# Kernel tuning notes

Measured on AMD Instinct MI355X. Metric: run time of the kernel, lower is better.

Reference implementation:

```python
import jax, jax.numpy as jnp
import numpy as np
from jax import lax

CURRICULUM_EP = 12
LI, LS, LW = 0.5, 0.8, 3.0


def _gauss_win(ws, C, dtype):
    coords = jnp.arange(ws, dtype=jnp.float32) - ws // 2
    g = jnp.exp(-coords ** 2 / (2 * 1.5 ** 2))
    win = g[None, :] * g[:, None]
    win = win / win.sum()
    # depthwise kernel, OIHW with I=1, O=C
    return jnp.broadcast_to(win[None, None], (C, 1, ws, ws)).astype(dtype)


def _dwconv(x, win, p, C):
    return lax.conv_general_dilated(
        x, win, window_strides=(1, 1), padding=[(p, p), (p, p)],
        dimension_numbers=('NCHW', 'OIHW', 'NCHW'), feature_group_count=C)


def diff_ssim(x, y, ws=11):
    C1, C2 = 0.01 ** 2, 0.03 ** 2
    C = x.shape[1]
    p = ws // 2
    win = _gauss_win(ws, C, x.dtype)
    mx = _dwconv(x, win, p, C)
    my = _dwconv(y, win, p, C)
    sxx = _dwconv(x * x, win, p, C) - mx ** 2
    syy = _dwconv(y * y, win, p, C) - my ** 2
    sxy = _dwconv(x * y, win, p, C) - mx * my
    ssim_map = (2 * mx * my + C1) * (2 * sxy + C2) / ((mx ** 2 + my ** 2 + C1) * (sxx + syy + C2))
    return ssim_map.mean()


def setup_inputs() -> dict:
    key = jax.random.key(0)
    k1, k2, k3, k4 = jax.random.split(key, 4)
    B, C, H, W = 16, 3, 512, 512
    NB = 1024  # watermark bits
    eps = 1e-4
    cover = jax.random.uniform(k1, (B, C, H, W), dtype=jnp.float32)
    wmed = jax.random.uniform(k2, (B, C, H, W), dtype=jnp.float32)
    wm_orig = jax.random.uniform(k3, (B, NB), dtype=jnp.float32)
    wm_ext = jnp.clip(jax.random.uniform(k4, (B, NB), dtype=jnp.float32), eps, 1.0 - eps)
    return {"cover": cover, "wmed": wmed, "wm_orig": wm_orig, "wm_ext": wm_ext, "epoch": 20}


def reference(cover, wmed, wm_orig, wm_ext, epoch):
    ml = jnp.mean((wmed - cover) ** 2)
    sv = diff_ssim(wmed, cover)
    sl = 1.0 - sv
    wl = jnp.mean(-(wm_orig * jnp.log(wm_ext) + (1.0 - wm_orig) * jnp.log(1.0 - wm_ext)))
    if epoch <= CURRICULUM_EP:
        w_img, w_ssim = 0.05, 0.05
    else:
        progress = min(1.0, (epoch - CURRICULUM_EP) / 10.0)
        w_img = 0.05 + (LI - 0.05) * progress
        w_ssim = 0.05 + (LS - 0.05) * progress
    total = w_img * ml + w_ssim * sl + LW * wl
    return (total, ml, sv, wl)
```

## Files before the change

kernel.cpp:

```cpp
#include <hip/hip_runtime.h>
#include <math.h>

#define H_IMG 512
#define W_IMG 512
#define TW 32
#define CH 32
#define NCHUNK 4
#define STRIP (CH*NCHUNK)
#define HALO 5
#define WS11 11
#define RING 42
#define RS 36
#define FSTR (RING*RS)
#define NTHREADS 256

typedef float f2 __attribute__((ext_vector_type(2)));

__host__ __device__ constexpr float WT(int t) {
    return (t==0||t==10) ? 0.00102838f :
           (t==1||t==9)  ? 0.00759873f :
           (t==2||t==8)  ? 0.03600075f :
           (t==3||t==7)  ? 0.10936070f :
           (t==4||t==6)  ? 0.21300556f :
           (t==5)        ? 0.26601172f : 0.0f;
}

static __device__ __forceinline__ f2 splat2(float v) { f2 r = {v, v}; return r; }

__global__ __launch_bounds__(NTHREADS, 5) void ssim_mse_tile(
        const float* __restrict__ cover, const float* __restrict__ wmed,
        float* __restrict__ part, int nParts) {
    __shared__ __align__(16) float rbuf[5*FSTR];

    const int tid = threadIdx.x;
    const int bx  = blockIdx.x & 15;
    const int ys  = (blockIdx.x >> 4) & 3;
    const int pl  = blockIdx.x >> 6;
    const size_t pbase = (size_t)pl * (H_IMG*W_IMG);
    const float* xp = wmed + pbase;
    const float* yp = cover + pbase;
    const int Y0  = ys << 7;
    const int tx0 = bx*TW - HALO;
    const bool xin = (bx != 0) && (bx != 15);

    float ssim_acc = 0.f, mse_acc = 0.f;

    for (int k = 0; k < NCHUNK; ++k) {
        const int nrows = (k == 0) ? (CH + 2*HALO) : CH;
        const int hr0   = (k == 0) ? -HALO : (CH*k + HALO);
        const int ntask = nrows << 3;

        for (int t = tid; t < ntask; t += NTHREADS) {
            const int r  = t >> 3, c0 = (t & 7) << 2;
            const int hr = hr0 + r;
            const int gy = Y0 + hr;
            const int slot = (hr + HALO) % RING;
            const bool rok = (unsigned)gy < (unsigned)H_IMG;
            float xv[14], yv[14];
            if (rok && xin) {
                const int ga = tx0 + c0 - 3;
                const float* rx = xp + (size_t)gy*W_IMG + ga;
                const float* ry = yp + (size_t)gy*W_IMG + ga;
                float4 XA = *(const float4*)(rx);
                float4 XB = *(const float4*)(rx + 4);
                float4 XC = *(const float4*)(rx + 8);
                float4 XD = *(const float4*)(rx + 12);
                float  XE = rx[16];
                float4 YA = *(const float4*)(ry);
                float4 YB = *(const float4*)(ry + 4);
                float4 YC = *(const float4*)(ry + 8);
                float4 YD = *(const float4*)(ry + 12);
                float  YE = ry[16];
                xv[0]=XA.w;  xv[1]=XB.x;  xv[2]=XB.y;  xv[3]=XB.z;  xv[4]=XB.w;
                xv[5]=XC.x;  xv[6]=XC.y;  xv[7]=XC.z;  xv[8]=XC.w;  xv[9]=XD.x;
                xv[10]=XD.y; xv[11]=XD.z; xv[12]=XD.w; xv[13]=XE;
                yv[0]=YA.w;  yv[1]=YB.x;  yv[2]=YB.y;  yv[3]=YB.z;  yv[4]=YB.w;
                yv[5]=YC.x;  yv[6]=YC.y;  yv[7]=YC.z;  yv[8]=YC.w;  yv[9]=YD.x;
                yv[10]=YD.y; yv[11]=YD.z; yv[12]=YD.w; yv[13]=YE;
            } else if (rok) {
                const int gc = tx0 + c0;
                const float* prx = xp + (size_t)gy*W_IMG + gc;
                const float* pry = yp + (size_t)gy*W_IMG + gc;
#pragma unroll
                for (int j = 0; j < 14; ++j) {
                    bool ok = (unsigned)(gc + j) < (unsigned)W_IMG;
                    xv[j] = ok ? prx[j] : 0.f;
                    yv[j] = ok ? pry[j] : 0.f;
                }
            } else {
#pragma unroll
                for (int j = 0; j < 14; ++j) { xv[j] = 0.f; yv[j] = 0.f; }
            }

            if ((unsigned)hr < (unsigned)STRIP) {
#pragma unroll
                for (int j = 5; j < 9; ++j) {
                    float d = xv[j] - yv[j];
                    mse_acc = fmaf(d, d, mse_acc);
                }
            }

            f2 A[5][2];
#pragma unroll
            for (int f = 0; f < 5; ++f) { A[f][0] = splat2(0.f); A[f][1] = splat2(0.f); }
#pragma unroll
            for (int j = 0; j < 14; ++j) {
                float px = xv[j], py = yv[j];
                float pxx = px*px, pyy = py*py, pxy = px*py;
#pragma unroll
                for (int p = 0; p < 2; ++p) {
                    const int t0 = j - 2*p;
                    if (t0 >= 0 && t0 <= WS11) {
                        const f2 wp = {WT(t0), WT(t0-1)};
                        A[0][p] = __builtin_elementwise_fma(wp, splat2(px),  A[0][p]);
                        A[1][p] = __builtin_elementwise_fma(wp, splat2(py),  A[1][p]);
                        A[2][p] = __builtin_elementwise_fma(wp, splat2(pxx), A[2][p]);
                        A[3][p] = __builtin_elementwise_fma(wp, splat2(pyy), A[3][p]);
                        A[4][p] = __builtin_elementwise_fma(wp, splat2(pxy), A[4][p]);
                    }
                }
            }
            float* wb = &rbuf[slot*RS + c0];
#pragma unroll
            for (int f = 0; f < 5; ++f) {
                *(float4*)(wb + f*FSTR) =
                    make_float4(A[f][0].x, A[f][0].y, A[f][1].x, A[f][1].y);
            }
        }
        __syncthreads();

        {
            const int c  = tid & 31;
            const int rg = tid >> 3 >> 2;
            const int sb = (CH*k + (rg << 2)) % RING;
            f2 acc[5][2];
#pragma unroll
            for (int f = 0; f < 5; ++f) {
                acc[f][0] = splat2(0.f); acc[f][1] = splat2(0.f);
            }
            const float* bp = rbuf + c;
#pragma unroll
            for (int i = 0; i < 14; ++i) {
                int sl = sb + i; if (sl >= RING) sl -= RING;
                const float* rp = bp + sl*RS;
#pragma unroll
                for (int f = 0; f < 5; ++f) {
                    float v = rp[f*FSTR];
#pragma unroll
                    for (int p = 0; p < 2; ++p) {
                        const int t0 = i - 2*p;
                        if (t0 >= 0 && t0 <= WS11) {
                            const f2 wp = {WT(t0), WT(t0-1)};
                            acc[f][p] = __builtin_elementwise_fma(wp, splat2(v), acc[f][p]);
                        }
                    }
                }
            }
            const f2 c1v = {1e-4f, 1e-4f};
            const f2 c2v = {9e-4f, 9e-4f};
            const f2 two = {2.f, 2.f};
#pragma unroll
            for (int p = 0; p < 2; ++p) {
                f2 mx = acc[0][p], my = acc[1][p];
                f2 sxx = acc[2][p] - mx*mx;
                f2 syy = acc[3][p] - my*my;
                f2 sxy = acc[4][p] - mx*my;
                f2 num = (two*mx*my + c1v) * (two*sxy + c2v);
                f2 den = (mx*mx + my*my + c1v) * (sxx + syy + c2v);
                ssim_acc += __fdividef(num.x, den.x) + __fdividef(num.y, den.y);
            }
        }
        __syncthreads();
    }

#pragma unroll
    for (int off = 32; off > 0; off >>= 1) {
        ssim_acc += __shfl_down(ssim_acc, off);
        mse_acc  += __shfl_down(mse_acc, off);
    }
    const int wid = tid >> 6, lane = tid & 63;
    if (lane == 0) { rbuf[wid] = ssim_acc; rbuf[4+wid] = mse_acc; }
    __syncthreads();
    if (tid == 0) {
        part[blockIdx.x] = rbuf[0]+rbuf[1]+rbuf[2]+rbuf[3];
        part[nParts + blockIdx.x] = rbuf[4]+rbuf[5]+rbuf[6]+rbuf[7];
    }
}

#define FT 1024
__global__ __launch_bounds__(FT) void finalize_k(
        const float* __restrict__ part, int nParts,
        const float* __restrict__ wm_orig, const float* __restrict__ wm_ext,
        int nWm, const int* __restrict__ epoch_p,
        float* __restrict__ out, double inv_npix, double inv_nwm) {
    __shared__ double red[48];
    int tid = threadIdx.x;
    double s_ssim = 0.0, s_mse = 0.0, s_wl = 0.0;
    const float4* s4 = (const float4*)part;
    const float4* m4 = (const float4*)(part + nParts);
    int n4 = nParts >> 2;
    for (int i = tid; i < n4; i += FT) {
        float4 v = s4[i];
        s_ssim += (double)((v.x + v.y) + (v.z + v.w));
        float4 u = m4[i];
        s_mse  += (double)((u.x + u.y) + (u.z + u.w));
    }
    const float4* p4 = (const float4*)wm_orig;
    const float4* q4 = (const float4*)wm_ext;
    int w4 = nWm >> 2;
    for (int i = tid; i < w4; i += FT) {
        float4 p = p4[i], q = q4[i];
        float a;
        a  = -(p.x*__logf(q.x) + (1.f-p.x)*__logf(1.f-q.x));
        a += -(p.y*__logf(q.y) + (1.f-p.y)*__logf(1.f-q.y));
        a += -(p.z*__logf(q.z) + (1.f-p.z)*__logf(1.f-q.z));
        a += -(p.w*__logf(q.w) + (1.f-p.w)*__logf(1.f-q.w));
        s_wl += (double)a;
    }
#pragma unroll
    for (int off = 32; off > 0; off >>= 1) {
        s_ssim += __shfl_down(s_ssim, off);
        s_mse  += __shfl_down(s_mse, off);
        s_wl   += __shfl_down(s_wl, off);
    }
    int wid = tid >> 6, lane = tid & 63;
    if (lane == 0) { red[wid] = s_ssim; red[16+wid] = s_mse; red[32+wid] = s_wl; }
    __syncthreads();
    if (tid == 0) {
        double ssim_sum = 0.0, mse_sum = 0.0, wl_sum = 0.0;
        for (int i = 0; i < 16; ++i) {
            ssim_sum += red[i]; mse_sum += red[16+i]; wl_sum += red[32+i];
        }
        float sv = (float)(ssim_sum * inv_npix);
        float ml = (float)(mse_sum  * inv_npix);
        float wl = (float)(wl_sum   * inv_nwm);
        int e = *epoch_p;
        float w_img, w_ssim;
        if (e <= 12) {
            w_img = 0.05f; w_ssim = 0.05f;
        } else {
            float progress = fminf(1.0f, (float)(e - 12) / 10.0f);
            w_img  = 0.05f + (0.5f - 0.05f)*progress;
            w_ssim = 0.05f + (0.8f - 0.05f)*progress;
        }
        float sl = 1.0f - sv;
        float total = w_img*ml + w_ssim*sl + 3.0f*wl;
        out[0] = total;
        out[1] = ml;
        out[2] = sv;
        out[3] = wl;
    }
}

extern "C" void kernel_launch(void* const* d_in, const int* in_sizes, int n_in,
                              void* d_out, int out_size, void* d_ws, size_t ws_size,
                              hipStream_t stream) {
    const float* cover   = (const float*)d_in[0];
    const float* wmed    = (const float*)d_in[1];
    const float* wm_orig = (const float*)d_in[2];
    const float* wm_ext  = (const float*)d_in[3];
    const int*   epoch   = (const int*)d_in[4];
    float* out = (float*)d_out;

    int npix   = in_sizes[0];
    int planes = npix / (H_IMG * W_IMG);
    int nWm    = in_sizes[2];

    int nBlocks = 16 * 4 * planes;
    int nParts  = nBlocks;
    float* part = (float*)d_ws;

    ssim_mse_tile<<<nBlocks, NTHREADS, 0, stream>>>(cover, wmed, part, nParts);
    finalize_k<<<1, FT, 0, stream>>>(part, nParts, wm_orig, wm_ext, nWm,
                                     epoch, out,
                                     1.0 / (double)npix, 1.0 / (double)nWm);
}
```

Measured before the change: 176.6 us.

## Prefetch next chunk's rows into registers while computing vertical SSIM pass

Restructures the per-chunk loop so global loads for the next chunk's rows are issued into registers before the vertical convolution and SSIM math of the current chunk, then consumed into the shared ring buffer afterward. The aim is to hide global memory latency behind compute. The prefetched row data raises register pressure, so launch bounds drop from 5 to 4 blocks per CU, reducing occupancy. The first chunk's 42 halo rows are also split explicitly over two load passes.

```diff
diff --git a/kernel.cpp b/kernel.cpp
--- a/kernel.cpp
+++ b/kernel.cpp
@@ -27,7 +27,105 @@
 
 static __device__ __forceinline__ f2 splat2(float v) { f2 r = {v, v}; return r; }
 
-__global__ __launch_bounds__(NTHREADS, 5) void ssim_mse_tile(
+struct Pre {
+    float4 XA, XB, XC, XD; float XE;
+    float4 YA, YB, YC, YD; float YE;
+};
+
+static __device__ __forceinline__ void issue_row(Pre& P,
+        const float* __restrict__ xp, const float* __restrict__ yp,
+        int gy, int tx0, int c0, bool xin, bool rok) {
+    if (!rok) return;
+    const size_t rowoff = (size_t)gy * W_IMG;
+    if (xin) {
+        const float* rx = xp + rowoff + (tx0 + c0 - 3);
+        const float* ry = yp + rowoff + (tx0 + c0 - 3);
+        P.XA = *(const float4*)(rx);
+        P.XB = *(const float4*)(rx + 4);
+        P.XC = *(const float4*)(rx + 8);
+        P.XD = *(const float4*)(rx + 12);
+        P.XE = rx[16];
+        P.YA = *(const float4*)(ry);
+        P.YB = *(const float4*)(ry + 4);
+        P.YC = *(const float4*)(ry + 8);
+        P.YD = *(const float4*)(ry + 12);
+        P.YE = ry[16];
+    } else {
+        const int gc = tx0 + c0;
+        const float* prx = xp + rowoff + gc;
+        const float* pry = yp + rowoff + gc;
+        float t[14], u[14];
+#pragma unroll
+        for (int j = 0; j < 14; ++j) {
+            bool ok = (unsigned)(gc + j) < (unsigned)W_IMG;
+            t[j] = ok ? prx[j] : 0.f;
+            u[j] = ok ? pry[j] : 0.f;
+        }
+        P.XA.w = t[0];
+        P.XB.x = t[1];  P.XB.y = t[2];  P.XB.z = t[3];  P.XB.w = t[4];
+        P.XC.x = t[5];  P.XC.y = t[6];  P.XC.z = t[7];  P.XC.w = t[8];
+        P.XD.x = t[9];  P.XD.y = t[10]; P.XD.z = t[11]; P.XD.w = t[12];
+        P.XE   = t[13];
+        P.YA.w = u[0];
+        P.YB.x = u[1];  P.YB.y = u[2];  P.YB.z = u[3];  P.YB.w = u[4];
+        P.YC.x = u[5];  P.YC.y = u[6];  P.YC.z = u[7];  P.YC.w = u[8];
+        P.YD.x = u[9];  P.YD.y = u[10]; P.YD.z = u[11]; P.YD.w = u[12];
+        P.YE   = u[13];
+    }
+}
+
+static __device__ __forceinline__ void consume_row(const Pre& P,
+        float* __restrict__ wb, bool rok, bool own, float& mse_acc) {
+    if (!rok) {
+        const float4 z = make_float4(0.f, 0.f, 0.f, 0.f);
+#pragma unroll
+        for (int f = 0; f < 5; ++f) *(float4*)(wb + f*FSTR) = z;
+        return;
+    }
+    float xv[14], yv[14];
+    xv[0]=P.XA.w;  xv[1]=P.XB.x;  xv[2]=P.XB.y;  xv[3]=P.XB.z;  xv[4]=P.XB.w;
+    xv[5]=P.XC.x;  xv[6]=P.XC.y;  xv[7]=P.XC.z;  xv[8]=P.XC.w;  xv[9]=P.XD.x;
+    xv[10]=P.XD.y; xv[11]=P.XD.z; xv[12]=P.XD.w; xv[13]=P.XE;
+    yv[0]=P.YA.w;  yv[1]=P.YB.x;  yv[2]=P.YB.y;  yv[3]=P.YB.z;  yv[4]=P.YB.w;
+    yv[5]=P.YC.x;  yv[6]=P.YC.y;  yv[7]=P.YC.z;  yv[8]=P.YC.w;  yv[9]=P.YD.x;
+    yv[10]=P.YD.y; yv[11]=P.YD.z; yv[12]=P.YD.w; yv[13]=P.YE;
+
+    if (own) {
+#pragma unroll
+        for (int j = 5; j < 9; ++j) {
+            float d = xv[j] - yv[j];
+            mse_acc = fmaf(d, d, mse_acc);
+        }
+    }
+
+    f2 A[5][2];
+#pragma unroll
+    for (int f = 0; f < 5; ++f) { A[f][0] = splat2(0.f); A[f][1] = splat2(0.f); }
+#pragma unroll
+    for (int j = 0; j < 14; ++j) {
+        float px = xv[j], py = yv[j];
+        float pxx = px*px, pyy = py*py, pxy = px*py;
+#pragma unroll
+        for (int p = 0; p < 2; ++p) {
+            const int t0 = j - 2*p;
+            if (t0 >= 0 && t0 <= WS11) {
+                const f2 wp = {WT(t0), WT(t0-1)};
+                A[0][p] = __builtin_elementwise_fma(wp, splat2(px),  A[0][p]);
+                A[1][p] = __builtin_elementwise_fma(wp, splat2(py),  A[1][p]);
+                A[2][p] = __builtin_elementwise_fma(wp, splat2(pxx), A[2][p]);
+                A[3][p] = __builtin_elementwise_fma(wp, splat2(pyy), A[3][p]);
+                A[4][p] = __builtin_elementwise_fma(wp, splat2(pxy), A[4][p]);
+            }
+        }
+    }
+#pragma unroll
+    for (int f = 0; f < 5; ++f) {
+        *(float4*)(wb + f*FSTR) =
+            make_float4(A[f][0].x, A[f][0].y, A[f][1].x, A[f][1].y);
+    }
+}
+
+__global__ __launch_bounds__(NTHREADS, 4) void ssim_mse_tile(
         const float* __restrict__ cover, const float* __restrict__ wmed,
         float* __restrict__ part, int nParts) {
     __shared__ __align__(16) float rbuf[5*FSTR];
@@ -43,96 +141,36 @@
     const int tx0 = bx*TW - HALO;
     const bool xin = (bx != 0) && (bx != 15);
 
+    const int rA = tid >> 3;
+    const int c0 = (tid & 7) << 2;
+
     float ssim_acc = 0.f, mse_acc = 0.f;
+    Pre P;
+
+    {
+        Pre P0, P1;
+        const int  hrA  = rA - HALO;
+        const int  gyA  = Y0 + hrA;
+        const bool rokA = (unsigned)gyA < (unsigned)H_IMG;
+        const bool two  = (tid < 80);
+        const int  gyB  = gyA + 32;
+        const bool rokB = two && ((unsigned)gyB < (unsigned)H_IMG);
+        issue_row(P0, xp, yp, gyA, tx0, c0, xin, rokA);
+        if (two) issue_row(P1, xp, yp, gyB, tx0, c0, xin, rokB);
+        consume_row(P0, &rbuf[rA*RS + c0], rokA, hrA >= 0, mse_acc);
+        if (two) consume_row(P1, &rbuf[(rA+32)*RS + c0], rokB, true, mse_acc);
+        const int  gy1  = Y0 + CH + HALO + rA;
+        const bool rok1 = (unsigned)gy1 < (unsigned)H_IMG;
+        issue_row(P, xp, yp, gy1, tx0, c0, xin, rok1);
+    }
+    __syncthreads();
+
+    int slotA = rA;
+    int sbB   = (tid >> 5) << 2;
 
     for (int k = 0; k < NCHUNK; ++k) {
-        const int nrows = (k == 0) ? (CH + 2*HALO) : CH;
-        const int hr0   = (k == 0) ? -HALO : (CH*k + HALO);
-        const int ntask = nrows << 3;
-
-        for (int t = tid; t < ntask; t += NTHREADS) {
-            const int r  = t >> 3, c0 = (t & 7) << 2;
-            const int hr = hr0 + r;
-            const int gy = Y0 + hr;
-            const int slot = (hr + HALO) % RING;
-            const bool rok = (unsigned)gy < (unsigned)H_IMG;
-            float xv[14], yv[14];
-            if (rok && xin) {
-                const int ga = tx0 + c0 - 3;
-                const float* rx = xp + (size_t)gy*W_IMG + ga;
-                const float* ry = yp + (size_t)gy*W_IMG + ga;
-                float4 XA = *(const float4*)(rx);
-                float4 XB = *(const float4*)(rx + 4);
-                float4 XC = *(const float4*)(rx + 8);
-                float4 XD = *(const float4*)(rx + 12);
-                float  XE = rx[16];
-                float4 YA = *(const float4*)(ry);
-                float4 YB = *(const float4*)(ry + 4);
-                float4 YC = *(const float4*)(ry + 8);
-                float4 YD = *(const float4*)(ry + 12);
-                float  YE = ry[16];
-                xv[0]=XA.w;  xv[1]=XB.x;  xv[2]=XB.y;  xv[3]=XB.z;  xv[4]=XB.w;
-                xv[5]=XC.x;  xv[6]=XC.y;  xv[7]=XC.z;  xv[8]=XC.w;  xv[9]=XD.x;
-                xv[10]=XD.y; xv[11]=XD.z; xv[12]=XD.w; xv[13]=XE;
-                yv[0]=YA.w;  yv[1]=YB.x;  yv[2]=YB.y;  yv[3]=YB.z;  yv[4]=YB.w;
-                yv[5]=YC.x;  yv[6]=YC.y;  yv[7]=YC.z;  yv[8]=YC.w;  yv[9]=YD.x;
-                yv[10]=YD.y; yv[11]=YD.z; yv[12]=YD.w; yv[13]=YE;
-            } else if (rok) {
-                const int gc = tx0 + c0;
-                const float* prx = xp + (size_t)gy*W_IMG + gc;
-                const float* pry = yp + (size_t)gy*W_IMG + gc;
-#pragma unroll
-                for (int j = 0; j < 14; ++j) {
-                    bool ok = (unsigned)(gc + j) < (unsigned)W_IMG;
-                    xv[j] = ok ? prx[j] : 0.f;
-                    yv[j] = ok ? pry[j] : 0.f;
-                }
-            } else {
-#pragma unroll
-                for (int j = 0; j < 14; ++j) { xv[j] = 0.f; yv[j] = 0.f; }
-            }
-
-            if ((unsigned)hr < (unsigned)STRIP) {
-#pragma unroll
-                for (int j = 5; j < 9; ++j) {
-                    float d = xv[j] - yv[j];
-                    mse_acc = fmaf(d, d, mse_acc);
-                }
-            }
-
-            f2 A[5][2];
-#pragma unroll
-            for (int f = 0; f < 5; ++f) { A[f][0] = splat2(0.f); A[f][1] = splat2(0.f); }
-#pragma unroll
-            for (int j = 0; j < 14; ++j) {
-                float px = xv[j], py = yv[j];
-                float pxx = px*px, pyy = py*py, pxy = px*py;
-#pragma unroll
-                for (int p = 0; p < 2; ++p) {
-                    const int t0 = j - 2*p;
-                    if (t0 >= 0 && t0 <= WS11) {
-                        const f2 wp = {WT(t0), WT(t0-1)};
-                        A[0][p] = __builtin_elementwise_fma(wp, splat2(px),  A[0][p]);
-                        A[1][p] = __builtin_elementwise_fma(wp, splat2(py),  A[1][p]);
-                        A[2][p] = __builtin_elementwise_fma(wp, splat2(pxx), A[2][p]);
-                        A[3][p] = __builtin_elementwise_fma(wp, splat2(pyy), A[3][p]);
-                        A[4][p] = __builtin_elementwise_fma(wp, splat2(pxy), A[4][p]);
-                    }
-                }
-            }
-            float* wb = &rbuf[slot*RS + c0];
-#pragma unroll
-            for (int f = 0; f < 5; ++f) {
-                *(float4*)(wb + f*FSTR) =
-                    make_float4(A[f][0].x, A[f][0].y, A[f][1].x, A[f][1].y);
-            }
-        }
-        __syncthreads();
-
         {
-            const int c  = tid & 31;
-            const int rg = tid >> 3 >> 2;
-            const int sb = (CH*k + (rg << 2)) % RING;
+            const int c = tid & 31;
             f2 acc[5][2];
 #pragma unroll
             for (int f = 0; f < 5; ++f) {
@@ -141,7 +179,7 @@
             const float* bp = rbuf + c;
 #pragma unroll
             for (int i = 0; i < 14; ++i) {
-                int sl = sb + i; if (sl >= RING) sl -= RING;
+                int sl = sbB + i; if (sl >= RING) sl -= RING;
                 const float* rp = bp + sl*RS;
 #pragma unroll
                 for (int f = 0; f < 5; ++f) {
@@ -158,20 +196,36 @@
             }
             const f2 c1v = {1e-4f, 1e-4f};
             const f2 c2v = {9e-4f, 9e-4f};
-            const f2 two = {2.f, 2.f};
+            const f2 two2 = {2.f, 2.f};
 #pragma unroll
             for (int p = 0; p < 2; ++p) {
                 f2 mx = acc[0][p], my = acc[1][p];
                 f2 sxx = acc[2][p] - mx*mx;
                 f2 syy = acc[3][p] - my*my;
                 f2 sxy = acc[4][p] - mx*my;
-                f2 num = (two*mx*my + c1v) * (two*sxy + c2v);
+                f2 num = (two2*mx*my + c1v) * (two2*sxy + c2v);
                 f2 den = (mx*mx + my*my + c1v) * (sxx + syy + c2v);
                 ssim_acc += __fdividef(num.x, den.x) + __fdividef(num.y, den.y);
             }
         }
-        __syncthreads();
-    }
+
+        if (k + 1 < NCHUNK) {
+            __syncthreads();
+            const int  hr  = CH*(k+1) + HALO + rA;
+            const int  gy  = Y0 + hr;
+            const bool rok = (unsigned)gy < (unsigned)H_IMG;
+            consume_row(P, &rbuf[slotA*RS + c0], rok, hr < STRIP, mse_acc);
+            if (k + 2 < NCHUNK) {
+                const int  gy2  = gy + CH;
+                const bool rok2 = (unsigned)gy2 < (unsigned)H_IMG;
+                issue_row(P, xp, yp, gy2, tx0, c0, xin, rok2);
+            }
+            slotA += CH; if (slotA >= RING) slotA -= RING;
+            sbB   += CH; if (sbB   >= RING) sbB   -= RING;
+            __syncthreads();
+        }
+    }
+    __syncthreads();
 
 #pragma unroll
     for (int off = 32; off > 0; off >>= 1) {
```

Measured after the change: 198.8 us. 12.5% more time.

## Prefetch next chunk rows into registers and overlap loads with vertical pass

Applied to the files above, without the earlier changes.

Restructures the strip loop so each thread register-prefetches the global rows for the next chunk while the vertical convolution and SSIM of the current chunk run. The prologue fills the halo rows separately, and the per-chunk horizontal pass now reads the prefetched registers. Barriers become a custom s_waitcnt lgkmcnt plus s_barrier, and the occupancy hint drops from 5 to 4 waves to make room for the extra live registers. The aim is to hide global load latency behind compute, at the cost of more register pressure and lower occupancy.

```diff
diff --git a/kernel.cpp b/kernel.cpp
--- a/kernel.cpp
+++ b/kernel.cpp
@@ -16,6 +16,11 @@
 
 typedef float f2 __attribute__((ext_vector_type(2)));
 
+#define BAR() do { \
+    asm volatile("s_waitcnt lgkmcnt(0)" ::: "memory"); \
+    __builtin_amdgcn_s_barrier(); \
+} while (0)
+
 __host__ __device__ constexpr float WT(int t) {
     return (t==0||t==10) ? 0.00102838f :
            (t==1||t==9)  ? 0.00759873f :
@@ -27,7 +32,7 @@
 
 static __device__ __forceinline__ f2 splat2(float v) { f2 r = {v, v}; return r; }
 
-__global__ __launch_bounds__(NTHREADS, 5) void ssim_mse_tile(
+__global__ __launch_bounds__(NTHREADS, 4) void ssim_mse_tile(
         const float* __restrict__ cover, const float* __restrict__ wmed,
         float* __restrict__ part, int nParts) {
     __shared__ __align__(16) float rbuf[5*FSTR];
@@ -43,40 +48,166 @@
     const int tx0 = bx*TW - HALO;
     const bool xin = (bx != 0) && (bx != 15);
 
+    const int rA  = tid >> 3;
+    const int c0  = (tid & 7) << 2;
+    const int cB  = tid & 31;
+    const int rgB = tid >> 5;
+
     float ssim_acc = 0.f, mse_acc = 0.f;
+    float4 pXA, pXB, pXC, pXD, pYA, pYB, pYC, pYD;
+    float  pXE, pYE;
+
+    for (int t = tid; t < 336; t += NTHREADS) {
+        const int r  = t >> 3, cc = (t & 7) << 2;
+        const int hr = r - HALO;
+        const int gy = Y0 + hr;
+        const bool rok = (unsigned)gy < (unsigned)H_IMG;
+        float xv[14], yv[14];
+        if (rok && xin) {
+            const float* rx = xp + (size_t)gy*W_IMG + (tx0 + cc - 3);
+            const float* ry = yp + (size_t)gy*W_IMG + (tx0 + cc - 3);
+            float4 XA = *(const float4*)(rx);
+            float4 XB = *(const float4*)(rx + 4);
+            float4 XC = *(const float4*)(rx + 8);
+            float4 XD = *(const float4*)(rx + 12);
+            float  XE = rx[16];
+            float4 YA = *(const float4*)(ry);
+            float4 YB = *(const float4*)(ry + 4);
+            float4 YC = *(const float4*)(ry + 8);
+            float4 YD = *(const float4*)(ry + 12);
+            float  YE = ry[16];
+            xv[0]=XA.w;  xv[1]=XB.x;  xv[2]=XB.y;  xv[3]=XB.z;  xv[4]=XB.w;
+            xv[5]=XC.x;  xv[6]=XC.y;  xv[7]=XC.z;  xv[8]=XC.w;  xv[9]=XD.x;
+            xv[10]=XD.y; xv[11]=XD.z; xv[12]=XD.w; xv[13]=XE;
+            yv[0]=YA.w;  yv[1]=YB.x;  yv[2]=YB.y;  yv[3]=YB.z;  yv[4]=YB.w;
+            yv[5]=YC.x;  yv[6]=YC.y;  yv[7]=YC.z;  yv[8]=YC.w;  yv[9]=YD.x;
+            yv[10]=YD.y; yv[11]=YD.z; yv[12]=YD.w; yv[13]=YE;
+        } else if (rok) {
+            const int gc = tx0 + cc;
+            const float* prx = xp + (size_t)gy*W_IMG + gc;
+            const float* pry = yp + (size_t)gy*W_IMG + gc;
+#pragma unroll
+            for (int j = 0; j < 14; ++j) {
+                bool ok = (unsigned)(gc + j) < (unsigned)W_IMG;
+                xv[j] = ok ? prx[j] : 0.f;
+                yv[j] = ok ? pry[j] : 0.f;
+            }
+        } else {
+#pragma unroll
+            for (int j = 0; j < 14; ++j) { xv[j] = 0.f; yv[j] = 0.f; }
+        }
+        if ((unsigned)hr < (unsigned)STRIP) {
+#pragma unroll
+            for (int j = 5; j < 9; ++j) {
+                float d = xv[j] - yv[j];
+                mse_acc = fmaf(d, d, mse_acc);
+            }
+        }
+        f2 A[5][2];
+#pragma unroll
+        for (int f = 0; f < 5; ++f) { A[f][0] = splat2(0.f); A[f][1] = splat2(0.f); }
+#pragma unroll
+        for (int j = 0; j < 14; ++j) {
+            float px = xv[j], py = yv[j];
+            float pxx = px*px, pyy = py*py, pxy = px*py;
+#pragma unroll
+            for (int p = 0; p < 2; ++p) {
+                const int t0 = j - 2*p;
+                if (t0 >= 0 && t0 <= WS11) {
+                    const f2 wp = {WT(t0), WT(t0-1)};
+                    A[0][p] = __builtin_elementwise_fma(wp, splat2(px),  A[0][p]);
+                    A[1][p] = __builtin_elementwise_fma(wp, splat2(py),  A[1][p]);
+                    A[2][p] = __builtin_elementwise_fma(wp, splat2(pxx), A[2][p]);
+                    A[3][p] = __builtin_elementwise_fma(wp, splat2(pyy), A[3][p]);
+                    A[4][p] = __builtin_elementwise_fma(wp, splat2(pxy), A[4][p]);
+                }
+            }
+        }
+        float* wb = &rbuf[r*RS + cc];
+#pragma unroll
+        for (int f = 0; f < 5; ++f) {
+            *(float4*)(wb + f*FSTR) =
+                make_float4(A[f][0].x, A[f][0].y, A[f][1].x, A[f][1].y);
+        }
+    }
+    if (xin) {
+        const int gy1 = Y0 + CH + HALO + rA;
+        const float* rx = xp + (size_t)gy1*W_IMG + (tx0 + c0 - 3);
+        const float* ry = yp + (size_t)gy1*W_IMG + (tx0 + c0 - 3);
+        pXA = *(const float4*)(rx);
+        pXB = *(const float4*)(rx + 4);
+        pXC = *(const float4*)(rx + 8);
+        pXD = *(const float4*)(rx + 12);
+        pXE = rx[16];
+        pYA = *(const float4*)(ry);
+        pYB = *(const float4*)(ry + 4);
+        pYC = *(const float4*)(ry + 8);
+        pYD = *(const float4*)(ry + 12);
+        pYE = ry[16];
+    }
+    BAR();
+
+    int slotA = rA;
+    int sbB   = rgB << 2;
 
     for (int k = 0; k < NCHUNK; ++k) {
-        const int nrows = (k == 0) ? (CH + 2*HALO) : CH;
-        const int hr0   = (k == 0) ? -HALO : (CH*k + HALO);
-        const int ntask = nrows << 3;
-
-        for (int t = tid; t < ntask; t += NTHREADS) {
-            const int r  = t >> 3, c0 = (t & 7) << 2;
-            const int hr = hr0 + r;
-            const int gy = Y0 + hr;
-            const int slot = (hr + HALO) % RING;
-            const bool rok = (unsigned)gy < (unsigned)H_IMG;
+        {
+            f2 acc[5][2];
+#pragma unroll
+            for (int f = 0; f < 5; ++f) {
+                acc[f][0] = splat2(0.f); acc[f][1] = splat2(0.f);
+            }
+            const float* bp = rbuf + cB;
+#pragma unroll
+            for (int i = 0; i < 14; ++i) {
+                int sl = sbB + i; if (sl >= RING) sl -= RING;
+                const float* rp = bp + sl*RS;
+#pragma unroll
+                for (int f = 0; f < 5; ++f) {
+                    float v = rp[f*FSTR];
+#pragma unroll
+                    for (int p = 0; p < 2; ++p) {
+                        const int t0 = i - 2*p;
+                        if (t0 >= 0 && t0 <= WS11) {
+                            const f2 wp = {WT(t0), WT(t0-1)};
+                            acc[f][p] = __builtin_elementwise_fma(wp, splat2(v), acc[f][p]);
+                        }
+                    }
+                }
+            }
+            const f2 c1v = {1e-4f, 1e-4f};
+            const f2 c2v = {9e-4f, 9e-4f};
+            const f2 two2 = {2.f, 2.f};
+#pragma unroll
+            for (int p = 0; p < 2; ++p) {
+                f2 mx = acc[0][p], my = acc[1][p];
+                f2 sxx = acc[2][p] - mx*mx;
+                f2 syy = acc[3][p] - my*my;
+                f2 sxy = acc[4][p] - mx*my;
+                f2 num = (two2*mx*my + c1v) * (two2*sxy + c2v);
+                f2 den = (mx*mx + my*my + c1v) * (sxx + syy + c2v);
+                ssim_acc += __fdividef(num.x, den.x) + __fdividef(num.y, den.y);
+            }
+        }
+
+        if (k + 1 < NCHUNK) {
+            BAR();
+            const int  hr  = CH*(k+1) + HALO + rA;
+            const int  gy  = Y0 + hr;
+            const bool rok = gy < H_IMG;
             float xv[14], yv[14];
-            if (rok && xin) {
-                const int ga = tx0 + c0 - 3;
-                const float* rx = xp + (size_t)gy*W_IMG + ga;
-                const float* ry = yp + (size_t)gy*W_IMG + ga;
-                float4 XA = *(const float4*)(rx);
-                float4 XB = *(const float4*)(rx + 4);
-                float4 XC = *(const float4*)(rx + 8);
-                float4 XD = *(const float4*)(rx + 12);
-                float  XE = rx[16];
-                float4 YA = *(const float4*)(ry);
-                float4 YB = *(const float4*)(ry + 4);
-                float4 YC = *(const float4*)(ry + 8);
-                float4 YD = *(const float4*)(ry + 12);
-                float  YE = ry[16];
-                xv[0]=XA.w;  xv[1]=XB.x;  xv[2]=XB.y;  xv[3]=XB.z;  xv[4]=XB.w;
-                xv[5]=XC.x;  xv[6]=XC.y;  xv[7]=XC.z;  xv[8]=XC.w;  xv[9]=XD.x;
-                xv[10]=XD.y; xv[11]=XD.z; xv[12]=XD.w; xv[13]=XE;
-                yv[0]=YA.w;  yv[1]=YB.x;  yv[2]=YB.y;  yv[3]=YB.z;  yv[4]=YB.w;
-                yv[5]=YC.x;  yv[6]=YC.y;  yv[7]=YC.z;  yv[8]=YC.w;  yv[9]=YD.x;
-                yv[10]=YD.y; yv[11]=YD.z; yv[12]=YD.w; yv[13]=YE;
+            if (xin) {
+                xv[0]=pXA.w;  xv[1]=pXB.x;  xv[2]=pXB.y;  xv[3]=pXB.z;  xv[4]=pXB.w;
+                xv[5]=pXC.x;  xv[6]=pXC.y;  xv[7]=pXC.z;  xv[8]=pXC.w;  xv[9]=pXD.x;
+                xv[10]=pXD.y; xv[11]=pXD.z; xv[12]=pXD.w; xv[13]=pXE;
+                yv[0]=pYA.w;  yv[1]=pYB.x;  yv[2]=pYB.y;  yv[3]=pYB.z;  yv[4]=pYB.w;
+                yv[5]=pYC.x;  yv[6]=pYC.y;  yv[7]=pYC.z;  yv[8]=pYC.w;  yv[9]=pYD.x;
+                yv[10]=pYD.y; yv[11]=pYD.z; yv[12]=pYD.w; yv[13]=pYE;
+#pragma unroll
+                for (int j = 0; j < 14; ++j) {
+                    xv[j] = rok ? xv[j] : 0.f;
+                    yv[j] = rok ? yv[j] : 0.f;
+                }
             } else if (rok) {
                 const int gc = tx0 + c0;
                 const float* prx = xp + (size_t)gy*W_IMG + gc;
@@ -91,15 +222,13 @@
 #pragma unroll
                 for (int j = 0; j < 14; ++j) { xv[j] = 0.f; yv[j] = 0.f; }
             }
-
-            if ((unsigned)hr < (unsigned)STRIP) {
+            if (hr < STRIP) {
 #pragma unroll
                 for (int j = 5; j < 9; ++j) {
                     float d = xv[j] - yv[j];
                     mse_acc = fmaf(d, d, mse_acc);
                 }
             }
-
             f2 A[5][2];
 #pragma unroll
             for (int f = 0; f < 5; ++f) { A[f][0] = splat2(0.f); A[f][1] = splat2(0.f); }
@@ -120,58 +249,34 @@
                     }
                 }
             }
-            float* wb = &rbuf[slot*RS + c0];
+            float* wb = &rbuf[slotA*RS + c0];
 #pragma unroll
             for (int f = 0; f < 5; ++f) {
                 *(float4*)(wb + f*FSTR) =
                     make_float4(A[f][0].x, A[f][0].y, A[f][1].x, A[f][1].y);
             }
-        }
-        __syncthreads();
-
-        {
-            const int c  = tid & 31;
-            const int rg = tid >> 3 >> 2;
-            const int sb = (CH*k + (rg << 2)) % RING;
-            f2 acc[5][2];
-#pragma unroll
-            for (int f = 0; f < 5; ++f) {
-                acc[f][0] = splat2(0.f); acc[f][1] = splat2(0.f);
-            }
-            const float* bp = rbuf + c;
-#pragma unroll
-            for (int i = 0; i < 14; ++i) {
-                int sl = sb + i; if (sl >= RING) sl -= RING;
-                const float* rp = bp + sl*RS;
-#pragma unroll
-                for (int f = 0; f < 5; ++f) {
-                    float v = rp[f*FSTR];
-#pragma unroll
-                    for (int p = 0; p < 2; ++p) {
-                        const int t0 = i - 2*p;
-                        if (t0 >= 0 && t0 <= WS11) {
-                            const f2 wp = {WT(t0), WT(t0-1)};
-                            acc[f][p] = __builtin_elementwise_fma(wp, splat2(v), acc[f][p]);
-                        }
-                    }
-                }
-            }
-            const f2 c1v = {1e-4f, 1e-4f};
-            const f2 c2v = {9e-4f, 9e-4f};
-            const f2 two = {2.f, 2.f};
-#pragma unroll
-            for (int p = 0; p < 2; ++p) {
-                f2 mx = acc[0][p], my = acc[1][p];
-                f2 sxx = acc[2][p] - mx*mx;
-                f2 syy = acc[3][p] - my*my;
-                f2 sxy = acc[4][p] - mx*my;
-                f2 num = (two*mx*my + c1v) * (two*sxy + c2v);
-                f2 den = (mx*mx + my*my + c1v) * (sxx + syy + c2v);
-                ssim_acc += __fdividef(num.x, den.x) + __fdividef(num.y, den.y);
-            }
-        }
-        __syncthreads();
-    }
+            if (k + 2 < NCHUNK && xin) {
+                int gy2 = gy + CH;
+                if (gy2 > H_IMG-1) gy2 = H_IMG-1;
+                const float* rx = xp + (size_t)gy2*W_IMG + (tx0 + c0 - 3);
+                const float* ry = yp + (size_t)gy2*W_IMG + (tx0 + c0 - 3);
+                pXA = *(const float4*)(rx);
+                pXB = *(const float4*)(rx + 4);
+                pXC = *(const float4*)(rx + 8);
+                pXD = *(const float4*)(rx + 12);
+                pXE = rx[16];
+                pYA = *(const float4*)(ry);
+                pYB = *(const float4*)(ry + 4);
+                pYC = *(const float4*)(ry + 8);
+                pYD = *(const float4*)(ry + 12);
+                pYE = ry[16];
+            }
+            slotA += CH; if (slotA >= RING) slotA -= RING;
+            sbB   += CH; if (sbB   >= RING) sbB   -= RING;
+            BAR();
+        }
+    }
+    __syncthreads();
 
 #pragma unroll
     for (int off = 32; off > 0; off >>= 1) {
```

After: 534.8 us. 203% more time.

## Give each wavefront its own strip and LDS ring to remove block barriers

Applied to the files above, without the earlier changes.

Each block now covers a full-height column tile, and each of its four wavefronts owns a 128-row strip with a private 18-slot LDS ring. Each wavefront interleaves horizontal-conv production of 8 rows with vertical conv and SSIM over 8 output rows. Because a wavefront's LDS accesses stay in order, the per-chunk __syncthreads pairs go away and each wave streams through its strip independently. The grid shrinks fourfold, occupancy hints drop to 3, and correctness depends on wavefront-synchronous LDS ordering without explicit barriers.

```diff
diff --git a/kernel.cpp b/kernel.cpp
--- a/kernel.cpp
+++ b/kernel.cpp
@@ -4,14 +4,13 @@
 #define H_IMG 512
 #define W_IMG 512
 #define TW 32
-#define CH 32
-#define NCHUNK 4
-#define STRIP (CH*NCHUNK)
+#define STRIP 128
 #define HALO 5
 #define WS11 11
-#define RING 42
+#define RING 18
 #define RS 36
 #define FSTR (RING*RS)
+#define WLDS (5*FSTR)
 #define NTHREADS 256
 
 typedef float f2 __attribute__((ext_vector_type(2)));
@@ -27,118 +26,128 @@
 
 static __device__ __forceinline__ f2 splat2(float v) { f2 r = {v, v}; return r; }
 
-__global__ __launch_bounds__(NTHREADS, 5) void ssim_mse_tile(
+__global__ __launch_bounds__(NTHREADS, 3) void ssim_mse_tile(
         const float* __restrict__ cover, const float* __restrict__ wmed,
         float* __restrict__ part, int nParts) {
-    __shared__ __align__(16) float rbuf[5*FSTR];
-
-    const int tid = threadIdx.x;
-    const int bx  = blockIdx.x & 15;
-    const int ys  = (blockIdx.x >> 4) & 3;
-    const int pl  = blockIdx.x >> 6;
+    __shared__ __align__(16) float rbuf[4*WLDS];
+
+    const int tid  = threadIdx.x;
+    const int w    = tid >> 6;
+    const int lane = tid & 63;
+    const int bx   = blockIdx.x & 15;
+    const int pl   = blockIdx.x >> 4;
     const size_t pbase = (size_t)pl * (H_IMG*W_IMG);
     const float* xp = wmed + pbase;
     const float* yp = cover + pbase;
-    const int Y0  = ys << 7;
+    const int Y0  = w << 7;
     const int tx0 = bx*TW - HALO;
     const bool xin = (bx != 0) && (bx != 15);
+    float* ring = &rbuf[w*WLDS];
+
+    const int rL  = lane >> 3;
+    const int c0  = (lane & 7) << 2;
+    const int cB  = lane & 31;
+    const int rgB = lane >> 5;
 
     float ssim_acc = 0.f, mse_acc = 0.f;
 
-    for (int k = 0; k < NCHUNK; ++k) {
-        const int nrows = (k == 0) ? (CH + 2*HALO) : CH;
-        const int hr0   = (k == 0) ? -HALO : (CH*k + HALO);
-        const int ntask = nrows << 3;
-
-        for (int t = tid; t < ntask; t += NTHREADS) {
-            const int r  = t >> 3, c0 = (t & 7) << 2;
-            const int hr = hr0 + r;
-            const int gy = Y0 + hr;
-            const int slot = (hr + HALO) % RING;
-            const bool rok = (unsigned)gy < (unsigned)H_IMG;
-            float xv[14], yv[14];
-            if (rok && xin) {
-                const int ga = tx0 + c0 - 3;
-                const float* rx = xp + (size_t)gy*W_IMG + ga;
-                const float* ry = yp + (size_t)gy*W_IMG + ga;
-                float4 XA = *(const float4*)(rx);
-                float4 XB = *(const float4*)(rx + 4);
-                float4 XC = *(const float4*)(rx + 8);
-                float4 XD = *(const float4*)(rx + 12);
-                float  XE = rx[16];
-                float4 YA = *(const float4*)(ry);
-                float4 YB = *(const float4*)(ry + 4);
-                float4 YC = *(const float4*)(ry + 8);
-                float4 YD = *(const float4*)(ry + 12);
-                float  YE = ry[16];
-                xv[0]=XA.w;  xv[1]=XB.x;  xv[2]=XB.y;  xv[3]=XB.z;  xv[4]=XB.w;
-                xv[5]=XC.x;  xv[6]=XC.y;  xv[7]=XC.z;  xv[8]=XC.w;  xv[9]=XD.x;
-                xv[10]=XD.y; xv[11]=XD.z; xv[12]=XD.w; xv[13]=XE;
-                yv[0]=YA.w;  yv[1]=YB.x;  yv[2]=YB.y;  yv[3]=YB.z;  yv[4]=YB.w;
-                yv[5]=YC.x;  yv[6]=YC.y;  yv[7]=YC.z;  yv[8]=YC.w;  yv[9]=YD.x;
-                yv[10]=YD.y; yv[11]=YD.z; yv[12]=YD.w; yv[13]=YE;
-            } else if (rok) {
-                const int gc = tx0 + c0;
-                const float* prx = xp + (size_t)gy*W_IMG + gc;
-                const float* pry = yp + (size_t)gy*W_IMG + gc;
-#pragma unroll
-                for (int j = 0; j < 14; ++j) {
-                    bool ok = (unsigned)(gc + j) < (unsigned)W_IMG;
-                    xv[j] = ok ? prx[j] : 0.f;
-                    yv[j] = ok ? pry[j] : 0.f;
+    auto hconv_task = [&](int hr, int slot, int cc) {
+        const int gy = Y0 + hr;
+        const bool rok = (unsigned)gy < (unsigned)H_IMG;
+        float xv[14], yv[14];
+        if (rok && xin) {
+            const int ga = tx0 + cc - 3;
+            const float* rx = xp + (size_t)gy*W_IMG + ga;
+            const float* ry = yp + (size_t)gy*W_IMG + ga;
+            float4 XA = *(const float4*)(rx);
+            float4 XB = *(const float4*)(rx + 4);
+            float4 XC = *(const float4*)(rx + 8);
+            float4 XD = *(const float4*)(rx + 12);
+            float  XE = rx[16];
+            float4 YA = *(const float4*)(ry);
+            float4 YB = *(const float4*)(ry + 4);
+            float4 YC = *(const float4*)(ry + 8);
+            float4 YD = *(const float4*)(ry + 12);
+            float  YE = ry[16];
+            xv[0]=XA.w;  xv[1]=XB.x;  xv[2]=XB.y;  xv[3]=XB.z;  xv[4]=XB.w;
+            xv[5]=XC.x;  xv[6]=XC.y;  xv[7]=XC.z;  xv[8]=XC.w;  xv[9]=XD.x;
+            xv[10]=XD.y; xv[11]=XD.z; xv[12]=XD.w; xv[13]=XE;
+            yv[0]=YA.w;  yv[1]=YB.x;  yv[2]=YB.y;  yv[3]=YB.z;  yv[4]=YB.w;
+            yv[5]=YC.x;  yv[6]=YC.y;  yv[7]=YC.z;  yv[8]=YC.w;  yv[9]=YD.x;
+            yv[10]=YD.y; yv[11]=YD.z; yv[12]=YD.w; yv[13]=YE;
+        } else if (rok) {
+            const int gc = tx0 + cc;
+            const float* prx = xp + (size_t)gy*W_IMG + gc;
+            const float* pry = yp + (size_t)gy*W_IMG + gc;
+#pragma unroll
+            for (int j = 0; j < 14; ++j) {
+                bool ok = (unsigned)(gc + j) < (unsigned)W_IMG;
+                xv[j] = ok ? prx[j] : 0.f;
+                yv[j] = ok ? pry[j] : 0.f;
+            }
+        } else {
+#pragma unroll
+            for (int j = 0; j < 14; ++j) { xv[j] = 0.f; yv[j] = 0.f; }
+        }
+
+        if ((unsigned)hr < (unsigned)STRIP) {
+#pragma unroll
+            for (int j = 5; j < 9; ++j) {
+                float d = xv[j] - yv[j];
+                mse_acc = fmaf(d, d, mse_acc);
+            }
+        }
+
+        f2 A[5][2];
+#pragma unroll
+        for (int f = 0; f < 5; ++f) { A[f][0] = splat2(0.f); A[f][1] = splat2(0.f); }
+#pragma unroll
+        for (int j = 0; j < 14; ++j) {
+            float px = xv[j], py = yv[j];
+            float pxx = px*px, pyy = py*py, pxy = px*py;
+#pragma unroll
+            for (int p = 0; p < 2; ++p) {
+                const int t0 = j - 2*p;
+                if (t0 >= 0 && t0 <= WS11) {
+                    const f2 wp = {WT(t0), WT(t0-1)};
+                    A[0][p] = __builtin_elementwise_fma(wp, splat2(px),  A[0][p]);
+                    A[1][p] = __builtin_elementwise_fma(wp, splat2(py),  A[1][p]);
+                    A[2][p] = __builtin_elementwise_fma(wp, splat2(pxx), A[2][p]);
+                    A[3][p] = __builtin_elementwise_fma(wp, splat2(pyy), A[3][p]);
+                    A[4][p] = __builtin_elementwise_fma(wp, splat2(pxy), A[4][p]);
                 }
-            } else {
-#pragma unroll
-                for (int j = 0; j < 14; ++j) { xv[j] = 0.f; yv[j] = 0.f; }
-            }
-
-            if ((unsigned)hr < (unsigned)STRIP) {
-#pragma unroll
-                for (int j = 5; j < 9; ++j) {
-                    float d = xv[j] - yv[j];
-                    mse_acc = fmaf(d, d, mse_acc);
-                }
-            }
-
-            f2 A[5][2];
-#pragma unroll
-            for (int f = 0; f < 5; ++f) { A[f][0] = splat2(0.f); A[f][1] = splat2(0.f); }
-#pragma unroll
-            for (int j = 0; j < 14; ++j) {
-                float px = xv[j], py = yv[j];
-                float pxx = px*px, pyy = py*py, pxy = px*py;
-#pragma unroll
-                for (int p = 0; p < 2; ++p) {
-                    const int t0 = j - 2*p;
-                    if (t0 >= 0 && t0 <= WS11) {
-                        const f2 wp = {WT(t0), WT(t0-1)};
-                        A[0][p] = __builtin_elementwise_fma(wp, splat2(px),  A[0][p]);
-                        A[1][p] = __builtin_elementwise_fma(wp, splat2(py),  A[1][p]);
-                        A[2][p] = __builtin_elementwise_fma(wp, splat2(pxx), A[2][p]);
-                        A[3][p] = __builtin_elementwise_fma(wp, splat2(pyy), A[3][p]);
-                        A[4][p] = __builtin_elementwise_fma(wp, splat2(pxy), A[4][p]);
-                    }
-                }
-            }
-            float* wb = &rbuf[slot*RS + c0];
-#pragma unroll
-            for (int f = 0; f < 5; ++f) {
-                *(float4*)(wb + f*FSTR) =
-                    make_float4(A[f][0].x, A[f][0].y, A[f][1].x, A[f][1].y);
-            }
-        }
-        __syncthreads();
-
+            }
+        }
+        float* wb = &ring[slot*RS + cc];
+#pragma unroll
+        for (int f = 0; f < 5; ++f) {
+            *(float4*)(wb + f*FSTR) =
+                make_float4(A[f][0].x, A[f][0].y, A[f][1].x, A[f][1].y);
+        }
+    };
+
+    hconv_task((lane >> 3) - HALO, lane >> 3, (lane & 7) << 2);
+    if (lane < 16) {
+        const int t = lane + 64;
+        hconv_task((t >> 3) - HALO, t >> 3, (t & 7) << 2);
+    }
+
+    int sA = 10;
+    int sV = 0;
+    for (int k = 0; k < 16; ++k) {
         {
-            const int c  = tid & 31;
-            const int rg = tid >> 3 >> 2;
-            const int sb = (CH*k + (rg << 2)) % RING;
+            int slot = sA + rL; if (slot >= RING) slot -= RING;
+            hconv_task(8*k + HALO + rL, slot, c0);
+        }
+
+        {
+            int sb = sV + (rgB << 2); if (sb >= RING) sb -= RING;
             f2 acc[5][2];
 #pragma unroll
             for (int f = 0; f < 5; ++f) {
                 acc[f][0] = splat2(0.f); acc[f][1] = splat2(0.f);
             }
-            const float* bp = rbuf + c;
+            const float* bp = ring + cB;
 #pragma unroll
             for (int i = 0; i < 14; ++i) {
                 int sl = sb + i; if (sl >= RING) sl -= RING;
@@ -158,19 +167,21 @@
             }
             const f2 c1v = {1e-4f, 1e-4f};
             const f2 c2v = {9e-4f, 9e-4f};
-            const f2 two = {2.f, 2.f};
+            const f2 two2 = {2.f, 2.f};
 #pragma unroll
             for (int p = 0; p < 2; ++p) {
                 f2 mx = acc[0][p], my = acc[1][p];
                 f2 sxx = acc[2][p] - mx*mx;
                 f2 syy = acc[3][p] - my*my;
                 f2 sxy = acc[4][p] - mx*my;
-                f2 num = (two*mx*my + c1v) * (two*sxy + c2v);
+                f2 num = (two2*mx*my + c1v) * (two2*sxy + c2v);
                 f2 den = (mx*mx + my*my + c1v) * (sxx + syy + c2v);
                 ssim_acc += __fdividef(num.x, den.x) + __fdividef(num.y, den.y);
             }
         }
-        __syncthreads();
+
+        sA += 8; if (sA >= RING) sA -= RING;
+        sV += 8; if (sV >= RING) sV -= RING;
     }
 
 #pragma unroll
@@ -178,8 +189,8 @@
         ssim_acc += __shfl_down(ssim_acc, off);
         mse_acc  += __shfl_down(mse_acc, off);
     }
-    const int wid = tid >> 6, lane = tid & 63;
-    if (lane == 0) { rbuf[wid] = ssim_acc; rbuf[4+wid] = mse_acc; }
+    __syncthreads();
+    if (lane == 0) { rbuf[w] = ssim_acc; rbuf[4+w] = mse_acc; }
     __syncthreads();
     if (tid == 0) {
         part[blockIdx.x] = rbuf[0]+rbuf[1]+rbuf[2]+rbuf[3];
@@ -266,7 +277,7 @@
     int planes = npix / (H_IMG * W_IMG);
     int nWm    = in_sizes[2];
 
-    int nBlocks = 16 * 4 * planes;
+    int nBlocks = 16 * planes;
     int nParts  = nBlocks;
     float* part = (float*)d_ws;
 
```

Measured after the change: 173.7 us. Within noise of the previous version (-1.7%).
